# Kernel optimization log

Measured on AMD Instinct MI355X. Metric: run time of the kernel, lower is better.

## Reference

```python
import jax, jax.numpy as jnp
import numpy as np
from jax import lax

HEAD_DIM = 8          # attention_head_dim
EPS_ATTN = 1e-15
EPS_RMS = 1e-5
KPAD = 2              # kernel_size 5 -> padding 2


def setup_inputs() -> dict:
    key = jax.random.key(0)
    ks = jax.random.split(key, 9)
    B, C, H, W = 2, 1152, 64, 64
    inner = 1152                     # num_heads(144) * head_dim(8)
    ch3 = 3 * inner                  # 3456
    s = 0.02
    return {
        "hidden_states": jax.random.normal(ks[0], (B, C, H, W), jnp.float32),
        "Wq": jax.random.normal(ks[1], (inner, C), jnp.float32) * s,
        "Wk": jax.random.normal(ks[2], (inner, C), jnp.float32) * s,
        "Wv": jax.random.normal(ks[3], (inner, C), jnp.float32) * s,
        "proj_in_w": jax.random.normal(ks[4], (ch3, 1, 5, 5), jnp.float32) * s,   # depthwise 5x5
        "proj_out_w": jax.random.normal(ks[5], (ch3, HEAD_DIM, 1, 1), jnp.float32) * s,  # grouped 1x1, groups=3*heads
        "Wout": jax.random.normal(ks[6], (C, 2 * inner), jnp.float32) * s,
        "rms_w": jnp.ones((C,), jnp.float32),
        "rms_b": jnp.zeros((C,), jnp.float32),
    }


def reference(hidden_states, Wq, Wk, Wv, proj_in_w, proj_out_w, Wout, rms_w, rms_b):
    x = hidden_states
    B, C, H, W = x.shape
    xh = jnp.transpose(x, (0, 2, 3, 1))                      # BHWC
    q = xh @ Wq.T
    k = xh @ Wk.T
    v = xh @ Wv.T
    qkv = jnp.transpose(jnp.concatenate([q, k, v], axis=-1), (0, 3, 1, 2))  # B,3*inner,H,W
    ch = qkv.shape[1]
    # multiscale branch: depthwise 5x5 then grouped 1x1 (groups = 3*num_heads)
    ms = lax.conv_general_dilated(qkv, proj_in_w, (1, 1), [(KPAD, KPAD), (KPAD, KPAD)],
                                  dimension_numbers=("NCHW", "OIHW", "NCHW"),
                                  feature_group_count=ch)
    ms = lax.conv_general_dilated(ms, proj_out_w, (1, 1), [(0, 0), (0, 0)],
                                  dimension_numbers=("NCHW", "OIHW", "NCHW"),
                                  feature_group_count=ch // HEAD_DIM)
    hs = jnp.concatenate([qkv, ms], axis=1).astype(jnp.float32)   # B, 2*3*inner, H, W
    hs = hs.reshape(B, -1, 3 * HEAD_DIM, H * W)                   # B, G, 3d, N
    q2, k2, v2 = jnp.split(hs, 3, axis=2)                         # each B,G,d,N
    q2 = jax.nn.relu(q2)
    k2 = jax.nn.relu(k2)
    # linear attention: pad value with a ones row (for the normalizer)
    v_pad = jnp.concatenate([v2, jnp.ones_like(v2[:, :, :1])], axis=2)  # B,G,d+1,N
    scores = jnp.einsum("bgdn,bgen->bgde", v_pad, k2)             # B,G,d+1,d (tiny)
    out = jnp.einsum("bgde,bgen->bgdn", scores, q2)               # B,G,d+1,N
    out = out[:, :, :-1] / (out[:, :, -1:] + EPS_ATTN)            # normalize by last row
    out = out.reshape(B, -1, H, W)                                # B, 2*inner, H, W
    out = jnp.transpose(out, (0, 2, 3, 1)) @ Wout.T               # BHW,C_out
    # RMSNorm over channel (last) dim, with affine weight + bias
    ms2 = jnp.mean(out * out, axis=-1, keepdims=True)
    out = out * lax.rsqrt(ms2 + EPS_RMS) * rms_w + rms_b
    return jnp.transpose(out, (0, 3, 1, 2))
```

## Files before the change

kernel.cpp:

```cpp
#include <hip/hip_runtime.h>

typedef _Float16 f16;
typedef f16 f16x8 __attribute__((ext_vector_type(8)));
typedef float f32x16 __attribute__((ext_vector_type(16)));

#define NB 2
#define NC 1152
#define NHW 4096
#define NCH3 3456
#define NC2 2304

#define LO_SCALE 2048.0f
#define LO_INV (1.0f / 2048.0f)


__device__ __align__(16) f16 g_Wcat_h[(size_t)NCH3 * NC];
__device__ __align__(16) f16 g_Wcat_l[(size_t)NC * NC];
__device__ __align__(16) f16 g_WoutB_h[(size_t)NC * NC2];
__device__ __align__(16) f16 g_XT_h[(size_t)NB * NHW * NC];
__device__ __align__(16) f16 g_XT_l[(size_t)NB * NHW * NC];
__device__ __align__(16) f16 g_qkv[(size_t)NB * NCH3 * NHW];
__device__ __align__(16) f16 g_ms[(size_t)NB * NCH3 * NHW];
__device__ __align__(16) f16 g_attnT_h[(size_t)NB * NHW * NC2];
__device__ float g_part[NB * NHW];

__device__ __forceinline__ void gload16(const void* g, void* l) {
  __builtin_amdgcn_global_load_lds(
      (const __attribute__((address_space(1))) unsigned int*)g,
      (__attribute__((address_space(3))) unsigned int*)l, 16, 0, 0);
}

__device__ __forceinline__ void split_f16(float v, f16& h, f16& l) {
  h = (f16)v;
  l = (f16)((v - (float)h) * LO_SCALE);
}

__global__ __launch_bounds__(256) void convert_weights(
    const float* __restrict__ wq, const float* __restrict__ wk,
    const float* __restrict__ wv, const float* __restrict__ wout) {
  size_t idx = ((size_t)blockIdx.x * 256 + threadIdx.x) * 4;
  const size_t NWC = (size_t)NCH3 * NC;
  const size_t NWO = (size_t)NC * NC2;
  if (idx < NWC) {
    int p = (int)(idx / NC);
    int kk = (int)(idx % NC);
    int role = p / 1152, w = p % 1152;
    int g = w >> 3, r = w & 7;
    int c = g * 24 + role * 8 + r;
    const float* src = (c < 1152) ? wq + (size_t)c * NC + kk
                      : (c < 2304) ? wk + (size_t)(c - 1152) * NC + kk
                                   : wv + (size_t)(c - 2304) * NC + kk;
    if (p < 1152) {
#pragma unroll
      for (int j = 0; j < 4; ++j)
        split_f16(src[j], g_Wcat_h[idx + j], g_Wcat_l[idx + j]);
    } else {
#pragma unroll
      for (int j = 0; j < 4; ++j) g_Wcat_h[idx + j] = (f16)src[j];
    }
  } else {
    size_t k = idx - NWC;
    if (k < NWO) {
      const float* src = wout + k;
#pragma unroll
      for (int j = 0; j < 4; ++j) g_WoutB_h[k + j] = (f16)src[j];
    }
  }
}

__global__ __launch_bounds__(256) void transpose_x(const float* __restrict__ x) {
  __shared__ float tile[32][33];
  int z = blockIdx.z;
  int p0 = blockIdx.x * 32, c0 = blockIdx.y * 32;
  int tx = threadIdx.x, ty = threadIdx.y;
#pragma unroll
  for (int i = 0; i < 32; i += 8)
    tile[ty + i][tx] = x[((size_t)z * NC + c0 + ty + i) * NHW + p0 + tx];
  __syncthreads();
#pragma unroll
  for (int i = 0; i < 32; i += 8) {
    size_t o = ((size_t)z * NHW + p0 + ty + i) * NC + c0 + tx;
    split_f16(tile[tx][ty + i], g_XT_h[o], g_XT_l[o]);
  }
}

__global__ __launch_bounds__(512, 1) void gemm1s_kernel() {
  __shared__ __align__(16) char smem[147456];
  int bid = blockIdx.x;
  int swz = (bid & 7) * 36 + (bid >> 3);
  int bx = swz % 9, rem = swz / 9;
  int bm = bx * 128, bn = (rem & 15) * 256, bz = rem >> 4;

  const int tid = threadIdx.x;
  const int lane = tid & 63;
  const int wid = tid >> 6;
  const int wr = wid >> 2, wc = wid & 3;
  const size_t boff = (size_t)bz * ((size_t)NHW * NC);
  const f16* Bh = g_XT_h + boff;
  const f16* Bl = g_XT_l + boff;
  f16* Cb = g_qkv + (size_t)bz * ((size_t)NCH3 * NHW);
  const int srow = tid >> 2;
  const int skb = (((tid & 3) ^ ((srow >> 1) & 3)) * 8);
  const f16* gAh = g_Wcat_h + (size_t)(bm + srow) * NC + skb;
  const f16* gAl = g_Wcat_l + (size_t)(bm + srow) * NC + skb;
  const f16* gBh0 = Bh + (size_t)(bn + srow) * NC + skb;
  const f16* gBl0 = Bl + (size_t)(bn + srow) * NC + skb;
  const f16* gBh1 = Bh + (size_t)(bn + 128 + srow) * NC + skb;
  const f16* gBl1 = Bl + (size_t)(bn + 128 + srow) * NC + skb;
  const int ldso = tid * 16;

  f32x16 acc[2][2] = {};
  f32x16 acc2[2][2] = {};
  const int r31 = lane & 31;
  const int key = (r31 >> 1) & 3;
  const int kblk = lane >> 5;

#define BUF(b, off) (smem + (b) * 49152 + (off))
#define STAGE_S(buf, tile)                                      \
  do {                                                          \
    size_t ko = (size_t)(tile) * 32;                            \
    gload16(gAh + ko, BUF(buf, 0) + ldso);                      \
    gload16(gAl + ko, BUF(buf, 8192) + ldso);                   \
    gload16(gBh0 + ko, BUF(buf, 16384) + ldso);                 \
    gload16(gBh1 + ko, BUF(buf, 24576) + ldso);                 \
    gload16(gBl0 + ko, BUF(buf, 32768) + ldso);                 \
    gload16(gBl1 + ko, BUF(buf, 40960) + ldso);                 \
  } while (0)

#define COMPUTE_S(buf)                                                         \
  do {                                                                         \
    const f16* sAh = (const f16*)BUF(buf, 0);                                  \
    const f16* sAl = (const f16*)BUF(buf, 8192);                               \
    const f16* sBh = (const f16*)BUF(buf, 16384);                              \
    const f16* sBl = (const f16*)BUF(buf, 32768);                              \
    _Pragma("unroll") for (int kh = 0; kh < 2; ++kh) {                         \
      const int bsw = ((kh * 2 + kblk) ^ key) * 8;                             \
      f16x8 ah[2], al[2], bh[2], bl[2];                                        \
      _Pragma("unroll") for (int mb = 0; mb < 2; ++mb) {                       \
        int ro = (wr * 64 + mb * 32 + r31) * 32 + bsw;                         \
        ah[mb] = *(const f16x8*)(sAh + ro);                                    \
        al[mb] = *(const f16x8*)(sAl + ro);                                    \
      }                                                                        \
      _Pragma("unroll") for (int nb = 0; nb < 2; ++nb) {                       \
        int ro = (wc * 64 + nb * 32 + r31) * 32 + bsw;                         \
        bh[nb] = *(const f16x8*)(sBh + ro);                                    \
        bl[nb] = *(const f16x8*)(sBl + ro);                                    \
      }                                                                        \
      __builtin_amdgcn_s_setprio(1);                                           \
      _Pragma("unroll") for (int mb = 0; mb < 2; ++mb)                         \
        _Pragma("unroll") for (int nb = 0; nb < 2; ++nb) {                     \
          acc[mb][nb]  = __builtin_amdgcn_mfma_f32_32x32x16_f16(ah[mb], bh[nb], acc[mb][nb], 0, 0, 0);  \
          acc2[mb][nb] = __builtin_amdgcn_mfma_f32_32x32x16_f16(ah[mb], bl[nb], acc2[mb][nb], 0, 0, 0); \
          acc2[mb][nb] = __builtin_amdgcn_mfma_f32_32x32x16_f16(al[mb], bh[nb], acc2[mb][nb], 0, 0, 0); \
        }                                                                      \
      __builtin_amdgcn_s_setprio(0);                                           \
    }                                                                          \
  } while (0)

  const int NT = NC / 32;
  STAGE_S(0, 0);
  STAGE_S(1, 1);
  int cb = 0, sb = 2;
#pragma unroll 1
  for (int t = 0; t < NT - 1; ++t) {
    asm volatile("s_waitcnt vmcnt(6)" ::: "memory");
    __builtin_amdgcn_s_barrier();
    __builtin_amdgcn_sched_barrier(0);
    if (t + 2 < NT) STAGE_S(sb, t + 2);
    COMPUTE_S(cb);
    __builtin_amdgcn_sched_barrier(0);
    __builtin_amdgcn_s_barrier();
    cb = (cb == 2) ? 0 : cb + 1;
    sb = (sb == 2) ? 0 : sb + 1;
  }
  asm volatile("s_waitcnt vmcnt(0)" ::: "memory");
  __builtin_amdgcn_s_barrier();
  __builtin_amdgcn_sched_barrier(0);
  COMPUTE_S(cb);
#undef STAGE_S
#undef COMPUTE_S
#undef BUF
#pragma unroll
  for (int mb = 0; mb < 2; ++mb)
#pragma unroll
    for (int nb = 0; nb < 2; ++nb) {
      int col = bn + wc * 64 + nb * 32 + r31;
#pragma unroll
      for (int reg = 0; reg < 16; ++reg) {
        int row = bm + wr * 64 + mb * 32 + (reg & 3) + 8 * (reg >> 2) + 4 * (lane >> 5);
        Cb[(size_t)row * NHW + col] = (f16)(acc[mb][nb][reg] + acc2[mb][nb][reg] * LO_INV);
      }
    }
}

__global__ __launch_bounds__(512, 1) void gemm1p_kernel() {
  __shared__ __align__(16) f16 sA[3][256 * 32];
  __shared__ __align__(16) f16 sB[3][256 * 32];
  int bid = blockIdx.x;
  int swz = (bid & 7) * 36 + (bid >> 3);
  int bx = swz % 9, rem = swz / 9;
  int bmG = 1152 + bx * 256;
  int bn = (rem & 15) * 256;
  int bz = rem >> 4;

  const int tid = threadIdx.x;
  const int lane = tid & 63;
  const int wid = tid >> 6;
  const int wr = wid >> 2, wc = wid & 3;
  const f16* Bb = g_XT_h + (size_t)bz * ((size_t)NHW * NC);
  f16* Cb = g_qkv + (size_t)bz * ((size_t)NCH3 * NHW);
  const int srow = tid >> 2;
  const int skb = (((tid & 3) ^ ((srow >> 1) & 3)) * 8);
  const f16* gA0 = g_Wcat_h + (size_t)(bmG + srow) * NC + skb;
  const f16* gA1 = g_Wcat_h + (size_t)(bmG + 128 + srow) * NC + skb;
  const f16* gB0 = Bb + (size_t)(bn + srow) * NC + skb;
  const f16* gB1 = Bb + (size_t)(bn + 128 + srow) * NC + skb;
  const int ldso = tid * 16;

  f32x16 acc[4][2] = {};
  const int r31 = lane & 31;
  const int key = (r31 >> 1) & 3;
  const int kblk = lane >> 5;

#define STG_A(buf, tile)                                        \
  do {                                                          \
    size_t ko = (size_t)(tile) * 32;                            \
    gload16(gA0 + ko, (char*)sA[buf] + ldso);                   \
    gload16(gA1 + ko, (char*)sA[buf] + 8192 + ldso);            \
  } while (0)
#define STG_B(buf, tile)                                        \
  do {                                                          \
    size_t ko = (size_t)(tile) * 32;                            \
    gload16(gB0 + ko, (char*)sB[buf] + ldso);                   \
    gload16(gB1 + ko, (char*)sB[buf] + 8192 + ldso);            \
  } while (0)

#define FPHASE(buf, ks, STG)                                                   \
  do {                                                                         \
    STG;                                                                       \
    const int bsw = ((ks) * 2 + kblk) * 8;                                     \
    f16x8 af[4], bf[2];                                                        \
    _Pragma("unroll") for (int ma = 0; ma < 4; ++ma) {                         \
      int row = wr * 128 + ma * 32 + r31;                                      \
      af[ma] = *(const f16x8*)(sA[buf] + row * 32 + ((bsw >> 3) ^ key) * 8);   \
    }                                                                          \
    _Pragma("unroll") for (int nb = 0; nb < 2; ++nb) {                         \
      int row = wc * 64 + nb * 32 + r31;                                       \
      bf[nb] = *(const f16x8*)(sB[buf] + row * 32 + ((bsw >> 3) ^ key) * 8);   \
    }                                                                          \
    __builtin_amdgcn_s_setprio(1);                                             \
    _Pragma("unroll") for (int ma = 0; ma < 4; ++ma)                           \
      _Pragma("unroll") for (int nb = 0; nb < 2; ++nb)                         \
        acc[ma][nb] = __builtin_amdgcn_mfma_f32_32x32x16_f16(af[ma], bf[nb], acc[ma][nb], 0, 0, 0); \
    __builtin_amdgcn_s_setprio(0);                                             \
  } while (0)

  const int NT = NC / 32;
  STG_A(0, 0); STG_B(0, 0);
  STG_A(1, 1); STG_B(1, 1);
  int cb = 0;
#pragma unroll 1
  for (int t = 0; t < NT - 2; ++t) {
    asm volatile("s_waitcnt vmcnt(4)" ::: "memory");
    __builtin_amdgcn_s_barrier();
    int pb = cb + 2; if (pb >= 3) pb -= 3;
    FPHASE(cb, 0, STG_A(pb, t + 2));
    FPHASE(cb, 1, STG_B(pb, t + 2));
    cb = (cb == 2) ? 0 : cb + 1;
  }
  asm volatile("s_waitcnt vmcnt(4)" ::: "memory");
  __builtin_amdgcn_s_barrier();
  FPHASE(cb, 0, (void)0);
  FPHASE(cb, 1, (void)0);
  cb = (cb == 2) ? 0 : cb + 1;
  asm volatile("s_waitcnt vmcnt(0)" ::: "memory");
  __builtin_amdgcn_s_barrier();
  FPHASE(cb, 0, (void)0);
  FPHASE(cb, 1, (void)0);
#undef STG_A
#undef STG_B
#undef FPHASE
#pragma unroll
  for (int ma = 0; ma < 4; ++ma)
#pragma unroll
    for (int nb = 0; nb < 2; ++nb) {
      int col = bn + wc * 64 + nb * 32 + r31;
#pragma unroll
      for (int reg = 0; reg < 16; ++reg) {
        int row = bmG + wr * 128 + ma * 32 + (reg & 3) + 8 * (reg >> 2) + 4 * (lane >> 5);
        Cb[(size_t)row * NHW + col] = (f16)acc[ma][nb][reg];
      }
    }
}

template <int M, int N, int K>
__device__ __forceinline__ void gemm_body_plain(
    const f16* __restrict__ A, const f16* __restrict__ Bt,
    float* __restrict__ C, int bm, int bn, int bz) {
  __shared__ __align__(16) f16 sA[3][128 * 32];
  __shared__ __align__(16) f16 sB[3][128 * 32];
  const int tid = threadIdx.x;
  const int lane = tid & 63;
  const int wid = tid >> 6;
  const int wr = wid >> 1, wc = wid & 1;
  const f16* Bb = Bt + (size_t)bz * ((size_t)N * K);
  float* Cb = C + (size_t)bz * ((size_t)M * N);
  const int srow = tid >> 2;
  const int skb = (((tid & 3) ^ ((srow >> 1) & 3)) * 8);
  const f16* gA0 = A + (size_t)(bm + srow) * K + skb;
  const f16* gA1 = A + (size_t)(bm + 64 + srow) * K + skb;
  const f16* gB0 = Bb + (size_t)(bn + srow) * K + skb;
  const f16* gB1 = Bb + (size_t)(bn + 64 + srow) * K + skb;
  const int ldso = tid * 16;

  f32x16 acc[2][2] = {};
  const int r31 = lane & 31;
  const int key = (r31 >> 1) & 3;
  const int kblk = lane >> 5;

#define STAGE_P(buf, tile)                              \
  do {                                                  \
    size_t ko = (size_t)(tile) * 32;                    \
    gload16(gA0 + ko, (char*)sA[buf] + ldso);           \
    gload16(gA1 + ko, (char*)sA[buf] + 4096 + ldso);    \
    gload16(gB0 + ko, (char*)sB[buf] + ldso);           \
    gload16(gB1 + ko, (char*)sB[buf] + 4096 + ldso);    \
  } while (0)

#define COMPUTE_P(buf)                                                         \
  do {                                                                         \
    _Pragma("unroll") for (int kh = 0; kh < 2; ++kh) {                         \
      const int bsw = ((kh * 2 + kblk) ^ key) * 8;                             \
      f16x8 af[2], bf[2];                                                      \
      _Pragma("unroll") for (int mb = 0; mb < 2; ++mb)                         \
        af[mb] = *(const f16x8*)(sA[buf] + (wr * 64 + mb * 32 + r31) * 32 + bsw); \
      _Pragma("unroll") for (int nb = 0; nb < 2; ++nb)                         \
        bf[nb] = *(const f16x8*)(sB[buf] + (wc * 64 + nb * 32 + r31) * 32 + bsw); \
      __builtin_amdgcn_s_setprio(1);                                           \
      _Pragma("unroll") for (int mb = 0; mb < 2; ++mb)                         \
        _Pragma("unroll") for (int nb = 0; nb < 2; ++nb)                       \
          acc[mb][nb] = __builtin_amdgcn_mfma_f32_32x32x16_f16(af[mb], bf[nb], acc[mb][nb], 0, 0, 0); \
      __builtin_amdgcn_s_setprio(0);                                           \
    }                                                                          \
  } while (0)

  const int NT = K / 32;
  STAGE_P(0, 0);
  STAGE_P(1, 1);
  int cb = 0, sb = 2;
#pragma unroll 1
  for (int t = 0; t < NT - 1; ++t) {
    asm volatile("s_waitcnt vmcnt(4)" ::: "memory");
    __builtin_amdgcn_s_barrier();
    __builtin_amdgcn_sched_barrier(0);
    if (t + 2 < NT) STAGE_P(sb, t + 2);
    COMPUTE_P(cb);
    __builtin_amdgcn_sched_barrier(0);
    __builtin_amdgcn_s_barrier();
    cb = (cb == 2) ? 0 : cb + 1;
    sb = (sb == 2) ? 0 : sb + 1;
  }
  asm volatile("s_waitcnt vmcnt(0)" ::: "memory");
  __builtin_amdgcn_s_barrier();
  __builtin_amdgcn_sched_barrier(0);
  COMPUTE_P(cb);
#undef STAGE_P
#undef COMPUTE_P
#pragma unroll
  for (int nb = 0; nb < 2; ++nb) {
    int col = bn + wc * 64 + nb * 32 + r31;
    float csum = 0.f;
#pragma unroll
    for (int mb = 0; mb < 2; ++mb)
#pragma unroll
      for (int reg = 0; reg < 16; ++reg) {
        int row = bm + wr * 64 + mb * 32 + (reg & 3) + 8 * (reg >> 2) + 4 * (lane >> 5);
        float v = acc[mb][nb][reg];
        Cb[(size_t)row * N + col] = v;
        csum += v * v;
      }
    atomicAdd(&g_part[bz * NHW + col], csum);
  }
}

__global__ __launch_bounds__(256, 2) void gemm2_kernel(float* __restrict__ out) {
  int bid = blockIdx.x;
  int swz = (bid & 7) * (576 / 8) + (bid >> 3);
  int bx = swz % 9, rem = swz / 9;
  int by = rem & 31, bz = rem >> 5;
  gemm_body_plain<NC, NHW, NC2>(g_WoutB_h, g_attnT_h, out,
                                bx * 128, by * 128, bz);
}

__global__ __launch_bounds__(256) void conv_kernel(const float* __restrict__ wdw,
                                                   const float* __restrict__ wpw) {
  const int z = blockIdx.z, gg = blockIdx.y;
  const int pbase = (gg % 3) * 1152 + (gg / 3) * 8;
  const int px = blockIdx.x * 2048 + threadIdx.x * 8;
  const int h = px >> 6, w0 = px & 63;
  const f16* base = g_qkv + ((size_t)z * NCH3 + pbase) * NHW;

  float dw[8][8];
#pragma unroll
  for (int ci = 0; ci < 8; ++ci) {
    const float* wd = wdw + (gg * 8 + ci) * 25;
    const f16* srcc = base + (size_t)ci * NHW;
    float acc[8] = {};
#pragma unroll
    for (int dy = -2; dy <= 2; ++dy) {
      int hh = h + dy;
      if (hh < 0 || hh > 63) continue;
      const f16* row = srcc + hh * 64;
      f16x8 Lv = {}, Rv = {};
      if (w0 >= 8) Lv = *(const f16x8*)(row + w0 - 8);
      f16x8 Mv = *(const f16x8*)(row + w0);
      if (w0 <= 48) Rv = *(const f16x8*)(row + w0 + 8);
      float c[24];
#pragma unroll
      for (int i = 0; i < 8; ++i) {
        c[i] = (float)Lv[i];
        c[8 + i] = (float)Mv[i];
        c[16 + i] = (float)Rv[i];
      }
      const float* wrow = wd + (dy + 2) * 5;
#pragma unroll
      for (int dx = 0; dx < 5; ++dx) {
        float wv = wrow[dx];
#pragma unroll
        for (int j = 0; j < 8; ++j) acc[j] += c[6 + j + dx] * wv;
      }
    }
#pragma unroll
    for (int j = 0; j < 8; ++j) dw[ci][j] = acc[j];
  }
#pragma unroll
  for (int o = 0; o < 8; ++o) {
    const float* wp = wpw + (size_t)(gg * 8 + o) * 8;
    float out[8] = {};
#pragma unroll
    for (int i = 0; i < 8; ++i) {
      float wv = wp[i];
#pragma unroll
      for (int j = 0; j < 8; ++j) out[j] += wv * dw[i][j];
    }
    f16x8 ov;
#pragma unroll
    for (int j = 0; j < 8; ++j) ov[j] = (f16)out[j];
    *(f16x8*)(g_ms + ((size_t)z * NCH3 + pbase + o) * NHW + px) = ov;
  }
}

__global__ __launch_bounds__(256) void attn_kernel() {
  int g = blockIdx.x;
  int z = blockIdx.y;
  int tid = threadIdx.x;
  const f16* buf = (g < 144) ? g_qkv : g_ms;
  int gq = (g < 144) ? g : g - 144;
  const f16* qp = buf + ((size_t)z * NCH3 + gq * 8) * NHW;
  const f16* kp = buf + ((size_t)z * NCH3 + 1152 + gq * 8) * NHW;
  const f16* vp = buf + ((size_t)z * NCH3 + 2304 + gq * 8) * NHW;

  float s[9][8];
#pragma unroll
  for (int d = 0; d < 9; ++d)
#pragma unroll
    for (int e = 0; e < 8; ++e) s[d][e] = 0.f;

  for (int p0 = tid * 8; p0 < NHW; p0 += 2048) {
    f16x8 kx[8], vx[8];
#pragma unroll
    for (int e = 0; e < 8; ++e) kx[e] = *(const f16x8*)(kp + (size_t)e * NHW + p0);
#pragma unroll
    for (int d = 0; d < 8; ++d) vx[d] = *(const f16x8*)(vp + (size_t)d * NHW + p0);
#pragma unroll
    for (int j = 0; j < 8; ++j) {
      float kv[8], vv[8];
#pragma unroll
      for (int e = 0; e < 8; ++e) kv[e] = fmaxf((float)kx[e][j], 0.f);
#pragma unroll
      for (int d = 0; d < 8; ++d) vv[d] = (float)vx[d][j];
#pragma unroll
      for (int e = 0; e < 8; ++e) {
#pragma unroll
        for (int d = 0; d < 8; ++d) s[d][e] += vv[d] * kv[e];
        s[8][e] += kv[e];
      }
    }
  }
#pragma unroll
  for (int d = 0; d < 9; ++d)
#pragma unroll
    for (int e = 0; e < 8; ++e) {
      float v = s[d][e];
#pragma unroll
      for (int off = 32; off > 0; off >>= 1) v += __shfl_xor(v, off, 64);
      s[d][e] = v;
    }
  __shared__ float sred[4][72];
  __shared__ float sc[72];
  int w = tid >> 6, lane = tid & 63;
  if (lane == 0) {
#pragma unroll
    for (int d = 0; d < 9; ++d)
#pragma unroll
      for (int e = 0; e < 8; ++e) sred[w][d * 8 + e] = s[d][e];
  }
  __syncthreads();
  if (tid < 72) sc[tid] = sred[0][tid] + sred[1][tid] + sred[2][tid] + sred[3][tid];
  __syncthreads();
  float scl[9][8];
#pragma unroll
  for (int d = 0; d < 9; ++d)
#pragma unroll
    for (int e = 0; e < 8; ++e) scl[d][e] = sc[d * 8 + e];

  for (int p0 = tid * 8; p0 < NHW; p0 += 2048) {
    f16x8 qx[8];
#pragma unroll
    for (int e = 0; e < 8; ++e) qx[e] = *(const f16x8*)(qp + (size_t)e * NHW + p0);
#pragma unroll
    for (int j = 0; j < 8; ++j) {
      float qv[8];
#pragma unroll
      for (int e = 0; e < 8; ++e) qv[e] = fmaxf((float)qx[e][j], 0.f);
      float o[9];
#pragma unroll
      for (int d = 0; d < 9; ++d) {
        float a = 0.f;
#pragma unroll
        for (int e = 0; e < 8; ++e) a += scl[d][e] * qv[e];
        o[d] = a;
      }
      float r = 1.f / (o[8] + 1e-15f);
      f16x8 oh;
#pragma unroll
      for (int d = 0; d < 8; ++d) oh[d] = (f16)(o[d] * r);
      *(f16x8*)(g_attnT_h + ((size_t)z * NHW + p0 + j) * NC2 + g * 8) = oh;
    }
  }
}

__global__ __launch_bounds__(256) void rms_zero() {
  g_part[blockIdx.x * 256 + threadIdx.x] = 0.f;
}
__global__ __launch_bounds__(256) void rms_norm(float* __restrict__ y,
                                                const float* __restrict__ w,
                                                const float* __restrict__ b) {
  size_t i = ((size_t)blockIdx.x * 256 + threadIdx.x) * 4;
  float4 v = *(const float4*)(y + i);
  int p = (int)(i & (NHW - 1));
  int c = (int)((i >> 12) % NC);
  int z = (int)(i / ((size_t)NC * NHW));
  const float inv = 1.0f / NC;
  float wc = w[c], bc = b[c];
  const float* pp = &g_part[z * NHW + p];
  v.x = v.x * rsqrtf(pp[0] * inv + 1e-5f) * wc + bc;
  v.y = v.y * rsqrtf(pp[1] * inv + 1e-5f) * wc + bc;
  v.z = v.z * rsqrtf(pp[2] * inv + 1e-5f) * wc + bc;
  v.w = v.w * rsqrtf(pp[3] * inv + 1e-5f) * wc + bc;
  *(float4*)(y + i) = v;
}

extern "C" void kernel_launch(void* const* d_in, const int* in_sizes, int n_in,
                              void* d_out, int out_size, void* d_ws, size_t ws_size,
                              hipStream_t stream) {
  const float* x = (const float*)d_in[0];
  const float* wq = (const float*)d_in[1];
  const float* wk = (const float*)d_in[2];
  const float* wv = (const float*)d_in[3];
  const float* wdw = (const float*)d_in[4];
  const float* wpw = (const float*)d_in[5];
  const float* wout = (const float*)d_in[6];
  const float* rw = (const float*)d_in[7];
  const float* rb = (const float*)d_in[8];
  float* y = (float*)d_out;

  convert_weights<<<6480, 256, 0, stream>>>(wq, wk, wv, wout);
  transpose_x<<<dim3(128, 36, 2), dim3(32, 8), 0, stream>>>(x);
  gemm1s_kernel<<<288, 512, 0, stream>>>();
  gemm1p_kernel<<<288, 512, 0, stream>>>();
  conv_kernel<<<dim3(2, 432, 2), 256, 0, stream>>>(wdw, wpw);
  attn_kernel<<<dim3(288, 2), 256, 0, stream>>>();
  rms_zero<<<32, 256, 0, stream>>>();
  gemm2_kernel<<<576, 256, 0, stream>>>(y);
  rms_norm<<<9216, 256, 0, stream>>>(y, rw, rb);
}
```

Measured before the change: 476.1 us.

## Merge split and plain QKV GEMMs into one launch with phased prefetch pipelines

The split-precision Q GEMM and the plain K/V GEMM now run in one 576-block launch, with blocks dispatched by swizzled index to either path, so the two workloads can fill the GPU together and one tail is removed. The split GEMM and gemm2 drop their two barriers per iteration and instead interleave half of each next-tile prefetch with each k-phase of compute, following the scheme the plain GEMM already used. This is meant to cut launch gaps, tail imbalance and barrier stalls. The risk is mixing heterogeneous block costs within a single grid, and the tighter overlap depends on the vmcnt accounting staying correct.

```diff
diff --git a/kernel.cpp b/kernel.cpp
--- a/kernel.cpp
+++ b/kernel.cpp
@@ -84,13 +84,7 @@
   }
 }
 
-__global__ __launch_bounds__(512, 1) void gemm1s_kernel() {
-  __shared__ __align__(16) char smem[147456];
-  int bid = blockIdx.x;
-  int swz = (bid & 7) * 36 + (bid >> 3);
-  int bx = swz % 9, rem = swz / 9;
-  int bm = bx * 128, bn = (rem & 15) * 256, bz = rem >> 4;
-
+__device__ __forceinline__ void gemm1_split_deep(char* smem, int bm, int bn, int bz) {
   const int tid = threadIdx.x;
   const int lane = tid & 63;
   const int wid = tid >> 6;
@@ -115,71 +109,77 @@
   const int key = (r31 >> 1) & 3;
   const int kblk = lane >> 5;
 
-#define BUF(b, off) (smem + (b) * 49152 + (off))
-#define STAGE_S(buf, tile)                                      \
+#define BUFS(b, off) (smem + (b) * 49152 + (off))
+#define STG_S0(buf, tile)                                       \
   do {                                                          \
     size_t ko = (size_t)(tile) * 32;                            \
-    gload16(gAh + ko, BUF(buf, 0) + ldso);                      \
-    gload16(gAl + ko, BUF(buf, 8192) + ldso);                   \
-    gload16(gBh0 + ko, BUF(buf, 16384) + ldso);                 \
-    gload16(gBh1 + ko, BUF(buf, 24576) + ldso);                 \
-    gload16(gBl0 + ko, BUF(buf, 32768) + ldso);                 \
-    gload16(gBl1 + ko, BUF(buf, 40960) + ldso);                 \
-  } while (0)
-
-#define COMPUTE_S(buf)                                                         \
+    gload16(gAh + ko, BUFS(buf, 0) + ldso);                     \
+    gload16(gAl + ko, BUFS(buf, 8192) + ldso);                  \
+    gload16(gBh0 + ko, BUFS(buf, 16384) + ldso);                \
+  } while (0)
+#define STG_S1(buf, tile)                                       \
+  do {                                                          \
+    size_t ko = (size_t)(tile) * 32;                            \
+    gload16(gBh1 + ko, BUFS(buf, 24576) + ldso);                \
+    gload16(gBl0 + ko, BUFS(buf, 32768) + ldso);                \
+    gload16(gBl1 + ko, BUFS(buf, 40960) + ldso);                \
+  } while (0)
+
+#define FPH_S(buf, kh, STG)                                                    \
   do {                                                                         \
-    const f16* sAh = (const f16*)BUF(buf, 0);                                  \
-    const f16* sAl = (const f16*)BUF(buf, 8192);                               \
-    const f16* sBh = (const f16*)BUF(buf, 16384);                              \
-    const f16* sBl = (const f16*)BUF(buf, 32768);                              \
-    _Pragma("unroll") for (int kh = 0; kh < 2; ++kh) {                         \
-      const int bsw = ((kh * 2 + kblk) ^ key) * 8;                             \
-      f16x8 ah[2], al[2], bh[2], bl[2];                                        \
-      _Pragma("unroll") for (int mb = 0; mb < 2; ++mb) {                       \
-        int ro = (wr * 64 + mb * 32 + r31) * 32 + bsw;                         \
-        ah[mb] = *(const f16x8*)(sAh + ro);                                    \
-        al[mb] = *(const f16x8*)(sAl + ro);                                    \
+    STG;                                                                       \
+    const int bsw = (((kh) * 2 + kblk) ^ key) * 8;                             \
+    const f16* sAh = (const f16*)BUFS(buf, 0);                                 \
+    const f16* sAl = (const f16*)BUFS(buf, 8192);                              \
+    const f16* sBh = (const f16*)BUFS(buf, 16384);                             \
+    const f16* sBl = (const f16*)BUFS(buf, 32768);                             \
+    f16x8 ah[2], al[2], bh[2], bl[2];                                          \
+    _Pragma("unroll") for (int mb = 0; mb < 2; ++mb) {                         \
+      int ro = (wr * 64 + mb * 32 + r31) * 32 + bsw;                           \
+      ah[mb] = *(const f16x8*)(sAh + ro);                                      \
+      al[mb] = *(const f16x8*)(sAl + ro);                                      \
+    }                                                                          \
+    _Pragma("unroll") for (int nb = 0; nb < 2; ++nb) {                         \
+      int ro = (wc * 64 + nb * 32 + r31) * 32 + bsw;                           \
+      bh[nb] = *(const f16x8*)(sBh + ro);                                      \
+      bl[nb] = *(const f16x8*)(sBl + ro);                                      \
+    }                                                                          \
+    __builtin_amdgcn_s_setprio(1);                                             \
+    _Pragma("unroll") for (int mb = 0; mb < 2; ++mb)                           \
+      _Pragma("unroll") for (int nb = 0; nb < 2; ++nb) {                       \
+        acc[mb][nb]  = __builtin_amdgcn_mfma_f32_32x32x16_f16(ah[mb], bh[nb], acc[mb][nb], 0, 0, 0);  \
+        acc2[mb][nb] = __builtin_amdgcn_mfma_f32_32x32x16_f16(ah[mb], bl[nb], acc2[mb][nb], 0, 0, 0); \
+        acc2[mb][nb] = __builtin_amdgcn_mfma_f32_32x32x16_f16(al[mb], bh[nb], acc2[mb][nb], 0, 0, 0); \
       }                                                                        \
-      _Pragma("unroll") for (int nb = 0; nb < 2; ++nb) {                       \
-        int ro = (wc * 64 + nb * 32 + r31) * 32 + bsw;                         \
-        bh[nb] = *(const f16x8*)(sBh + ro);                                    \
-        bl[nb] = *(const f16x8*)(sBl + ro);                                    \
-      }                                                                        \
-      __builtin_amdgcn_s_setprio(1);                                           \
-      _Pragma("unroll") for (int mb = 0; mb < 2; ++mb)                         \
-        _Pragma("unroll") for (int nb = 0; nb < 2; ++nb) {                     \
-          acc[mb][nb]  = __builtin_amdgcn_mfma_f32_32x32x16_f16(ah[mb], bh[nb], acc[mb][nb], 0, 0, 0);  \
-          acc2[mb][nb] = __builtin_amdgcn_mfma_f32_32x32x16_f16(ah[mb], bl[nb], acc2[mb][nb], 0, 0, 0); \
-          acc2[mb][nb] = __builtin_amdgcn_mfma_f32_32x32x16_f16(al[mb], bh[nb], acc2[mb][nb], 0, 0, 0); \
-        }                                                                      \
-      __builtin_amdgcn_s_setprio(0);                                           \
-    }                                                                          \
+    __builtin_amdgcn_s_setprio(0);                                             \
   } while (0)
 
   const int NT = NC / 32;
-  STAGE_S(0, 0);
-  STAGE_S(1, 1);
-  int cb = 0, sb = 2;
+  STG_S0(0, 0); STG_S1(0, 0);
+  STG_S0(1, 1); STG_S1(1, 1);
+  int cb = 0;
 #pragma unroll 1
-  for (int t = 0; t < NT - 1; ++t) {
+  for (int t = 0; t < NT - 2; ++t) {
     asm volatile("s_waitcnt vmcnt(6)" ::: "memory");
     __builtin_amdgcn_s_barrier();
-    __builtin_amdgcn_sched_barrier(0);
-    if (t + 2 < NT) STAGE_S(sb, t + 2);
-    COMPUTE_S(cb);
-    __builtin_amdgcn_sched_barrier(0);
-    __builtin_amdgcn_s_barrier();
+    int pb = cb + 2; if (pb >= 3) pb -= 3;
+    FPH_S(cb, 0, STG_S0(pb, t + 2));
+    FPH_S(cb, 1, STG_S1(pb, t + 2));
     cb = (cb == 2) ? 0 : cb + 1;
-    sb = (sb == 2) ? 0 : sb + 1;
-  }
+  }
+  asm volatile("s_waitcnt vmcnt(6)" ::: "memory");
+  __builtin_amdgcn_s_barrier();
+  FPH_S(cb, 0, (void)0);
+  FPH_S(cb, 1, (void)0);
+  cb = (cb == 2) ? 0 : cb + 1;
   asm volatile("s_waitcnt vmcnt(0)" ::: "memory");
   __builtin_amdgcn_s_barrier();
-  __builtin_amdgcn_sched_barrier(0);
-  COMPUTE_S(cb);
-#undef STAGE_S
-#undef COMPUTE_S
-#undef BUF
+  FPH_S(cb, 0, (void)0);
+  FPH_S(cb, 1, (void)0);
+#undef STG_S0
+#undef STG_S1
+#undef FPH_S
+#undef BUFS
 #pragma unroll
   for (int mb = 0; mb < 2; ++mb)
 #pragma unroll
@@ -193,16 +193,9 @@
     }
 }
 
-__global__ __launch_bounds__(512, 1) void gemm1p_kernel() {
-  __shared__ __align__(16) f16 sA[3][256 * 32];
-  __shared__ __align__(16) f16 sB[3][256 * 32];
-  int bid = blockIdx.x;
-  int swz = (bid & 7) * 36 + (bid >> 3);
-  int bx = swz % 9, rem = swz / 9;
-  int bmG = 1152 + bx * 256;
-  int bn = (rem & 15) * 256;
-  int bz = rem >> 4;
-
+__device__ __forceinline__ void gemm1_plain_deep(char* smem, int bmG, int bn, int bz) {
+  f16* sA0 = (f16*)smem;
+  f16* sB0 = (f16*)(smem + 49152);
   const int tid = threadIdx.x;
   const int lane = tid & 63;
   const int wid = tid >> 6;
@@ -222,31 +215,32 @@
   const int key = (r31 >> 1) & 3;
   const int kblk = lane >> 5;
 
+#define SA(b) (sA0 + (b) * 8192)
+#define SB(b) (sB0 + (b) * 8192)
 #define STG_A(buf, tile)                                        \
   do {                                                          \
     size_t ko = (size_t)(tile) * 32;                            \
-    gload16(gA0 + ko, (char*)sA[buf] + ldso);                   \
-    gload16(gA1 + ko, (char*)sA[buf] + 8192 + ldso);            \
+    gload16(gA0 + ko, (char*)SA(buf) + ldso);                   \
+    gload16(gA1 + ko, (char*)SA(buf) + 8192 + ldso);            \
   } while (0)
 #define STG_B(buf, tile)                                        \
   do {                                                          \
     size_t ko = (size_t)(tile) * 32;                            \
-    gload16(gB0 + ko, (char*)sB[buf] + ldso);                   \
-    gload16(gB1 + ko, (char*)sB[buf] + 8192 + ldso);            \
-  } while (0)
-
-#define FPHASE(buf, ks, STG)                                                   \
+    gload16(gB0 + ko, (char*)SB(buf) + ldso);                   \
+    gload16(gB1 + ko, (char*)SB(buf) + 8192 + ldso);            \
+  } while (0)
+#define FPH_P(buf, ks, STG)                                                    \
   do {                                                                         \
     STG;                                                                       \
-    const int bsw = ((ks) * 2 + kblk) * 8;                                     \
+    const int bsw = (((ks) * 2 + kblk) ^ key) * 8;                             \
     f16x8 af[4], bf[2];                                                        \
     _Pragma("unroll") for (int ma = 0; ma < 4; ++ma) {                         \
       int row = wr * 128 + ma * 32 + r31;                                      \
-      af[ma] = *(const f16x8*)(sA[buf] + row * 32 + ((bsw >> 3) ^ key) * 8);   \
+      af[ma] = *(const f16x8*)(SA(buf) + row * 32 + bsw);                      \
     }                                                                          \
     _Pragma("unroll") for (int nb = 0; nb < 2; ++nb) {                         \
       int row = wc * 64 + nb * 32 + r31;                                       \
-      bf[nb] = *(const f16x8*)(sB[buf] + row * 32 + ((bsw >> 3) ^ key) * 8);   \
+      bf[nb] = *(const f16x8*)(SB(buf) + row * 32 + bsw);                      \
     }                                                                          \
     __builtin_amdgcn_s_setprio(1);                                             \
     _Pragma("unroll") for (int ma = 0; ma < 4; ++ma)                           \
@@ -264,22 +258,24 @@
     asm volatile("s_waitcnt vmcnt(4)" ::: "memory");
     __builtin_amdgcn_s_barrier();
     int pb = cb + 2; if (pb >= 3) pb -= 3;
-    FPHASE(cb, 0, STG_A(pb, t + 2));
-    FPHASE(cb, 1, STG_B(pb, t + 2));
+    FPH_P(cb, 0, STG_A(pb, t + 2));
+    FPH_P(cb, 1, STG_B(pb, t + 2));
     cb = (cb == 2) ? 0 : cb + 1;
   }
   asm volatile("s_waitcnt vmcnt(4)" ::: "memory");
   __builtin_amdgcn_s_barrier();
-  FPHASE(cb, 0, (void)0);
-  FPHASE(cb, 1, (void)0);
+  FPH_P(cb, 0, (void)0);
+  FPH_P(cb, 1, (void)0);
   cb = (cb == 2) ? 0 : cb + 1;
   asm volatile("s_waitcnt vmcnt(0)" ::: "memory");
   __builtin_amdgcn_s_barrier();
-  FPHASE(cb, 0, (void)0);
-  FPHASE(cb, 1, (void)0);
+  FPH_P(cb, 0, (void)0);
+  FPH_P(cb, 1, (void)0);
 #undef STG_A
 #undef STG_B
-#undef FPHASE
+#undef FPH_P
+#undef SA
+#undef SB
 #pragma unroll
   for (int ma = 0; ma < 4; ++ma)
 #pragma unroll
@@ -293,24 +289,40 @@
     }
 }
 
-template <int M, int N, int K>
-__device__ __forceinline__ void gemm_body_plain(
-    const f16* __restrict__ A, const f16* __restrict__ Bt,
-    float* __restrict__ C, int bm, int bn, int bz) {
+__global__ __launch_bounds__(512, 1) void gemm1_kernel() {
+  __shared__ __align__(16) char smem[147456];
+  int bid = blockIdx.x;
+  int swz = (bid & 7) * 72 + (bid >> 3);
+  if (swz < 288) {
+    int bx = swz % 9, rem = swz / 9;
+    gemm1_split_deep(smem, bx * 128, (rem & 15) * 256, rem >> 4);
+  } else {
+    int w2 = swz - 288;
+    int bx = w2 % 9, rem = w2 / 9;
+    gemm1_plain_deep(smem, 1152 + bx * 256, (rem & 15) * 256, rem >> 4);
+  }
+}
+
+__global__ __launch_bounds__(256, 2) void gemm2_kernel(float* __restrict__ out) {
   __shared__ __align__(16) f16 sA[3][128 * 32];
   __shared__ __align__(16) f16 sB[3][128 * 32];
+  int bid = blockIdx.x;
+  int swz = (bid & 7) * (576 / 8) + (bid >> 3);
+  int bx = swz % 9, rem = swz / 9;
+  int bm = bx * 128, bn = (rem & 31) * 128, bz = rem >> 5;
+
   const int tid = threadIdx.x;
   const int lane = tid & 63;
   const int wid = tid >> 6;
   const int wr = wid >> 1, wc = wid & 1;
-  const f16* Bb = Bt + (size_t)bz * ((size_t)N * K);
-  float* Cb = C + (size_t)bz * ((size_t)M * N);
+  const f16* Bb = g_attnT_h + (size_t)bz * ((size_t)NHW * NC2);
+  float* Cb = out + (size_t)bz * ((size_t)NC * NHW);
   const int srow = tid >> 2;
   const int skb = (((tid & 3) ^ ((srow >> 1) & 3)) * 8);
-  const f16* gA0 = A + (size_t)(bm + srow) * K + skb;
-  const f16* gA1 = A + (size_t)(bm + 64 + srow) * K + skb;
-  const f16* gB0 = Bb + (size_t)(bn + srow) * K + skb;
-  const f16* gB1 = Bb + (size_t)(bn + 64 + srow) * K + skb;
+  const f16* gA0 = g_WoutB_h + (size_t)(bm + srow) * NC2 + skb;
+  const f16* gA1 = g_WoutB_h + (size_t)(bm + 64 + srow) * NC2 + skb;
+  const f16* gB0 = Bb + (size_t)(bn + srow) * NC2 + skb;
+  const f16* gB1 = Bb + (size_t)(bn + 64 + srow) * NC2 + skb;
   const int ldso = tid * 16;
 
   f32x16 acc[2][2] = {};
@@ -318,54 +330,59 @@
   const int key = (r31 >> 1) & 3;
   const int kblk = lane >> 5;
 
-#define STAGE_P(buf, tile)                              \
+#define STG_A2(buf, tile)                               \
   do {                                                  \
     size_t ko = (size_t)(tile) * 32;                    \
     gload16(gA0 + ko, (char*)sA[buf] + ldso);           \
     gload16(gA1 + ko, (char*)sA[buf] + 4096 + ldso);    \
+  } while (0)
+#define STG_B2(buf, tile)                               \
+  do {                                                  \
+    size_t ko = (size_t)(tile) * 32;                    \
     gload16(gB0 + ko, (char*)sB[buf] + ldso);           \
     gload16(gB1 + ko, (char*)sB[buf] + 4096 + ldso);    \
   } while (0)
-
-#define COMPUTE_P(buf)                                                         \
+#define FPH_2(buf, ks, STG)                                                    \
   do {                                                                         \
-    _Pragma("unroll") for (int kh = 0; kh < 2; ++kh) {                         \
-      const int bsw = ((kh * 2 + kblk) ^ key) * 8;                             \
-      f16x8 af[2], bf[2];                                                      \
-      _Pragma("unroll") for (int mb = 0; mb < 2; ++mb)                         \
-        af[mb] = *(const f16x8*)(sA[buf] + (wr * 64 + mb * 32 + r31) * 32 + bsw); \
+    STG;                                                                       \
+    const int bsw = (((ks) * 2 + kblk) ^ key) * 8;                             \
+    f16x8 af[2], bf[2];                                                        \
+    _Pragma("unroll") for (int mb = 0; mb < 2; ++mb)                           \
+      af[mb] = *(const f16x8*)(sA[buf] + (wr * 64 + mb * 32 + r31) * 32 + bsw);\
+    _Pragma("unroll") for (int nb = 0; nb < 2; ++nb)                           \
+      bf[nb] = *(const f16x8*)(sB[buf] + (wc * 64 + nb * 32 + r31) * 32 + bsw);\
+    __builtin_amdgcn_s_setprio(1);                                             \
+    _Pragma("unroll") for (int mb = 0; mb < 2; ++mb)                           \
       _Pragma("unroll") for (int nb = 0; nb < 2; ++nb)                         \
-        bf[nb] = *(const f16x8*)(sB[buf] + (wc * 64 + nb * 32 + r31) * 32 + bsw); \
-      __builtin_amdgcn_s_setprio(1);                                           \
-      _Pragma("unroll") for (int mb = 0; mb < 2; ++mb)                         \
-        _Pragma("unroll") for (int nb = 0; nb < 2; ++nb)                       \
-          acc[mb][nb] = __builtin_amdgcn_mfma_f32_32x32x16_f16(af[mb], bf[nb], acc[mb][nb], 0, 0, 0); \
-      __builtin_amdgcn_s_setprio(0);                                           \
-    }                                                                          \
-  } while (0)
-
-  const int NT = K / 32;
-  STAGE_P(0, 0);
-  STAGE_P(1, 1);
-  int cb = 0, sb = 2;
+        acc[mb][nb] = __builtin_amdgcn_mfma_f32_32x32x16_f16(af[mb], bf[nb], acc[mb][nb], 0, 0, 0); \
+    __builtin_amdgcn_s_setprio(0);                                             \
+  } while (0)
+
+  const int NT = NC2 / 32;
+  STG_A2(0, 0); STG_B2(0, 0);
+  STG_A2(1, 1); STG_B2(1, 1);
+  int cb = 0;
 #pragma unroll 1
-  for (int t = 0; t < NT - 1; ++t) {
+  for (int t = 0; t < NT - 2; ++t) {
     asm volatile("s_waitcnt vmcnt(4)" ::: "memory");
     __builtin_amdgcn_s_barrier();
-    __builtin_amdgcn_sched_barrier(0);
-    if (t + 2 < NT) STAGE_P(sb, t + 2);
-    COMPUTE_P(cb);
-    __builtin_amdgcn_sched_barrier(0);
-    __builtin_amdgcn_s_barrier();
+    int pb = cb + 2; if (pb >= 3) pb -= 3;
+    FPH_2(cb, 0, STG_A2(pb, t + 2));
+    FPH_2(cb, 1, STG_B2(pb, t + 2));
     cb = (cb == 2) ? 0 : cb + 1;
-    sb = (sb == 2) ? 0 : sb + 1;
-  }
+  }
+  asm volatile("s_waitcnt vmcnt(4)" ::: "memory");
+  __builtin_amdgcn_s_barrier();
+  FPH_2(cb, 0, (void)0);
+  FPH_2(cb, 1, (void)0);
+  cb = (cb == 2) ? 0 : cb + 1;
   asm volatile("s_waitcnt vmcnt(0)" ::: "memory");
   __builtin_amdgcn_s_barrier();
-  __builtin_amdgcn_sched_barrier(0);
-  COMPUTE_P(cb);
-#undef STAGE_P
-#undef COMPUTE_P
+  FPH_2(cb, 0, (void)0);
+  FPH_2(cb, 1, (void)0);
+#undef STG_A2
+#undef STG_B2
+#undef FPH_2
 #pragma unroll
   for (int nb = 0; nb < 2; ++nb) {
     int col = bn + wc * 64 + nb * 32 + r31;
@@ -376,20 +393,11 @@
       for (int reg = 0; reg < 16; ++reg) {
         int row = bm + wr * 64 + mb * 32 + (reg & 3) + 8 * (reg >> 2) + 4 * (lane >> 5);
         float v = acc[mb][nb][reg];
-        Cb[(size_t)row * N + col] = v;
+        Cb[(size_t)row * NHW + col] = v;
         csum += v * v;
       }
     atomicAdd(&g_part[bz * NHW + col], csum);
   }
-}
-
-__global__ __launch_bounds__(256, 2) void gemm2_kernel(float* __restrict__ out) {
-  int bid = blockIdx.x;
-  int swz = (bid & 7) * (576 / 8) + (bid >> 3);
-  int bx = swz % 9, rem = swz / 9;
-  int by = rem & 31, bz = rem >> 5;
-  gemm_body_plain<NC, NHW, NC2>(g_WoutB_h, g_attnT_h, out,
-                                bx * 128, by * 128, bz);
 }
 
 __global__ __launch_bounds__(256) void conv_kernel(const float* __restrict__ wdw,
@@ -577,8 +585,7 @@
 
   convert_weights<<<6480, 256, 0, stream>>>(wq, wk, wv, wout);
   transpose_x<<<dim3(128, 36, 2), dim3(32, 8), 0, stream>>>(x);
-  gemm1s_kernel<<<288, 512, 0, stream>>>();
-  gemm1p_kernel<<<288, 512, 0, stream>>>();
+  gemm1_kernel<<<576, 512, 0, stream>>>();
   conv_kernel<<<dim3(2, 432, 2), 256, 0, stream>>>(wdw, wpw);
   attn_kernel<<<dim3(288, 2), 256, 0, stream>>>();
   rms_zero<<<32, 256, 0, stream>>>();
```

New measurement: 438.1 us. 8.0% less time.
